# Kernel tuning notes

Hardware: AMD Instinct MI355X
Metric: run time of the kernel (lower is better)

The kernel has to match this reference:

```python
import jax, jax.numpy as jnp
import numpy as np

DIM = 512
HEADS = 16
WS = (2, 7, 7)
N = WS[0] * WS[1] * WS[2]  # 98
NW = 64  # number of windows in mask
B_ = 512  # num_windows * batch
HEAD_DIM = DIM // HEADS
SCALE = HEAD_DIM ** -0.5
TABLE = (2 * WS[0] - 1) * (2 * WS[1] - 1) * (2 * WS[2] - 1)  # 507


def _relative_position_index():
    # Faithful to the repo (note: middle coord is NOT multiplied by (2*Ww-1),
    # matching the source exactly).
    ct, ch, cw = np.arange(WS[0]), np.arange(WS[1]), np.arange(WS[2])
    coords = np.stack(np.meshgrid(ct, ch, cw, indexing='ij'))  # [3,Th,Tw,Tw]
    flat = coords.reshape(3, -1)  # [3,N]
    rel = flat[:, :, None] - flat[:, None, :]  # [3,N,N]
    rel = rel.transpose(1, 2, 0).copy()  # [N,N,3]
    rel[:, :, 0] += WS[0] - 1
    rel[:, :, 1] += WS[1] - 1
    rel[:, :, 2] += WS[2] - 1
    rel[:, :, 0] *= (2 * WS[1] - 1) * (2 * WS[2] - 1)
    return rel.sum(-1).astype(np.int32)  # [N,N]


def setup_inputs() -> dict:
    key = jax.random.key(0)
    ks = jax.random.split(key, 7)
    x = jax.random.normal(ks[0], (B_, N, DIM), dtype=jnp.float32)
    mask = jnp.zeros((NW, N, N), dtype=jnp.float32)
    qkv_w = jax.random.normal(ks[1], (3 * DIM, DIM), dtype=jnp.float32) * (DIM ** -0.5)
    qkv_b = jnp.zeros((3 * DIM,), dtype=jnp.float32)
    proj_w = jax.random.normal(ks[2], (DIM, DIM), dtype=jnp.float32) * (DIM ** -0.5)
    proj_b = jnp.zeros((DIM,), dtype=jnp.float32)
    bias_table = jax.random.normal(ks[3], (TABLE, HEADS), dtype=jnp.float32) * 0.02
    rel_index = jnp.asarray(_relative_position_index())
    return {"x": x, "mask": mask, "qkv_w": qkv_w, "qkv_b": qkv_b,
            "proj_w": proj_w, "proj_b": proj_b, "bias_table": bias_table,
            "rel_index": rel_index}


def reference(x, mask, qkv_w, qkv_b, proj_w, proj_b, bias_table, rel_index):
    Bw, n, c = x.shape
    # QKV projection -> [3, B_, H, N, hd]
    qkv = (x @ qkv_w.T + qkv_b).reshape(Bw, n, 3, HEADS, HEAD_DIM)
    qkv = qkv.transpose(2, 0, 3, 1, 4)
    q, k, v = qkv[0], qkv[1], qkv[2]
    attn = jnp.einsum('bhnd,bhmd->bhnm', q * SCALE, k)  # [B_,H,N,N]
    # Gathered relative position bias -> [H,N,N]
    bias = bias_table[rel_index.reshape(-1)].reshape(n, n, HEADS).transpose(2, 0, 1)
    attn = attn + bias[None]
    # Broadcast mask over batch groups of nW windows
    nW = mask.shape[0]
    attn = attn.reshape(Bw // nW, nW, HEADS, n, n) + mask[None, :, None]
    attn = attn.reshape(Bw, HEADS, n, n)
    attn = jax.nn.softmax(attn, axis=-1)
    out = jnp.einsum('bhnm,bhmd->bhnd', attn, v)
    out = out.transpose(0, 2, 1, 3).reshape(Bw, n, c)
    return out @ proj_w.T + proj_b
```

## Files before the change

### kernel.cpp

```cpp
#include <hip/hip_runtime.h>
#include <stdint.h>

#define HEADS 16
#define NTOK 98
#define HD 32
#define SCALE_Q 0.17677669529663687f

typedef __attribute__((ext_vector_type(4))) float floatx4;
typedef __attribute__((ext_vector_type(8))) short shortx8;

__device__ __forceinline__ unsigned short f2bf(float f) {
  union { float f; unsigned u; } v; v.f = f;
  unsigned r = v.u + 0x7fffu + ((v.u >> 16) & 1u);
  return (unsigned short)(r >> 16);
}
__device__ __forceinline__ float bf2f(unsigned short s) {
  union { unsigned u; float f; } v; v.u = ((unsigned)s) << 16;
  return v.f;
}

__device__ __forceinline__ void gload_lds16(const void* g, void* l) {
  __builtin_amdgcn_global_load_lds(
      (const __attribute__((address_space(1))) unsigned int*)g,
      (__attribute__((address_space(3))) unsigned int*)l, 16, 0, 0);
}

__global__ void convert_x_kernel(const float* __restrict__ x,
                                 unsigned short* __restrict__ xbf) {
  int idx = blockIdx.x * 256 + threadIdx.x;
  const float4 f0 = *(const float4*)(x + (size_t)idx * 8);
  const float4 f1 = *(const float4*)(x + (size_t)idx * 8 + 4);
  union { ushort us[8]; uint4 u4; } pk;
  pk.us[0] = f2bf(f0.x); pk.us[1] = f2bf(f0.y);
  pk.us[2] = f2bf(f0.z); pk.us[3] = f2bf(f0.w);
  pk.us[4] = f2bf(f1.x); pk.us[5] = f2bf(f1.y);
  pk.us[6] = f2bf(f1.z); pk.us[7] = f2bf(f1.w);
  *(uint4*)(xbf + (size_t)idx * 8) = pk.u4;
}

__global__ void convert_w_kernel(const float* __restrict__ qkv_w,
                                 const float* __restrict__ proj_w,
                                 unsigned short* __restrict__ wq,
                                 unsigned short* __restrict__ wp) {
  int idx = blockIdx.x * 256 + threadIdx.x;
  if (idx < 1536 * 512) wq[idx] = f2bf(qkv_w[idx]);
  if (idx < 512 * 512) wp[idx] = f2bf(proj_w[idx]);
}

__global__ void bmprep_kernel(const float* __restrict__ table,
                              const int* __restrict__ rel,
                              const float* __restrict__ mask,
                              unsigned short* __restrict__ biasF,
                              unsigned short* __restrict__ maskF) {
  int idx = blockIdx.x * 256 + threadIdx.x;
  if (idx < 229376) {
    int e = idx & 31, lane = (idx >> 5) & 63;
    int rest = idx >> 11;
    int mt = rest % 7, h = rest / 7;
    int nt = e >> 2, r = e & 3;
    int i = mt * 16 + ((lane >> 4) << 2) + r;
    int j = (nt << 4) + (lane & 15);
    int ii = i < NTOK ? i : 97, jj = j < NTOK ? j : 97;
    float v = (nt < 7) ? table[rel[ii * NTOK + jj] * HEADS + h] : 0.f;
    biasF[idx] = f2bf(v);
  } else {
    int t = idx - 229376;
    int e = t & 31, lane = (t >> 5) & 63;
    int rest = t >> 11;
    int mt = rest % 7, wdx = rest / 7;
    int nt = e >> 2, r = e & 3;
    int i = mt * 16 + ((lane >> 4) << 2) + r;
    int j = (nt << 4) + (lane & 15);
    float v;
    if (nt >= 7) v = 0.f;
    else if (j >= NTOK) v = -1e30f;
    else {
      int ii = i < NTOK ? i : 97;
      v = mask[wdx * (NTOK * NTOK) + ii * NTOK + j];
    }
    maskF[t] = f2bf(v);
  }
}

__global__ __launch_bounds__(512, 2)
void qkv_gemm_kernel(const unsigned short* __restrict__ xbf,
                     const unsigned short* __restrict__ wbf,
                     const float* __restrict__ qkv_b,
                     unsigned short* __restrict__ q_out,
                     unsigned short* __restrict__ k_out,
                     unsigned short* __restrict__ v_out) {
  __shared__ unsigned short As[3][128 * 32];
  __shared__ unsigned short Bs[3][256 * 32];
  const int tid = threadIdx.x;
  const int wave = tid >> 6, lane = tid & 63;
  const int m0 = blockIdx.x * 128, n0 = blockIdx.y * 256;
  const int wm = wave & 1, wn = wave >> 1;
  const int ln15 = lane & 15, qd = lane >> 4;
  const int bl_r = lane >> 2, bl_s = lane & 3;

  const int sg_st = bl_s ^ ((bl_r >> 1) & 3);
  const int swz_rd = (qd ^ ((ln15 >> 1) & 3)) * 8;

  const unsigned short* aG = xbf + (size_t)(m0 + wave * 16 + bl_r) * 512 + sg_st * 8;
  const unsigned short* bG0 = wbf + (size_t)(n0 + wave * 32 + bl_r) * 512 + sg_st * 8;
  const unsigned short* bG1 = wbf + (size_t)(n0 + wave * 32 + 16 + bl_r) * 512 + sg_st * 8;

#define QSTAGE(bufi, kk)                                                        \
  do {                                                                          \
    gload_lds16((const void*)(aG + (kk)), (void*)&As[bufi][wave * 512]);        \
    gload_lds16((const void*)(bG0 + (kk)), (void*)&Bs[bufi][wave * 1024]);      \
    gload_lds16((const void*)(bG1 + (kk)), (void*)&Bs[bufi][wave * 1024 + 512]);\
  } while (0)

  QSTAGE(0, 0);
  QSTAGE(1, 32);

  floatx4 acc[4][4] = {};
#pragma unroll
  for (int it = 0; it < 16; ++it) {
    if (it == 15) asm volatile("s_waitcnt vmcnt(0)" ::: "memory");
    else          asm volatile("s_waitcnt vmcnt(3)" ::: "memory");
    __builtin_amdgcn_sched_barrier(0);
    __builtin_amdgcn_s_barrier();
    __builtin_amdgcn_sched_barrier(0);
    if (it + 2 < 16) QSTAGE((it + 2) % 3, (it + 2) * 32);
    const unsigned short* Ab = As[it % 3];
    const unsigned short* Bb = Bs[it % 3];
    shortx8 afrag[4], bfrag[4];
#pragma unroll
    for (int mt = 0; mt < 4; ++mt)
      afrag[mt] = *(const shortx8*)&Ab[(wm * 64 + mt * 16 + ln15) * 32 + swz_rd];
#pragma unroll
    for (int nt = 0; nt < 4; ++nt)
      bfrag[nt] = *(const shortx8*)&Bb[(wn * 64 + nt * 16 + ln15) * 32 + swz_rd];
#pragma unroll
    for (int mt = 0; mt < 4; ++mt)
#pragma unroll
      for (int nt = 0; nt < 4; ++nt)
        acc[mt][nt] = __builtin_amdgcn_mfma_f32_16x16x32_bf16(
            afrag[mt], bfrag[nt], acc[mt][nt], 0, 0, 0);
  }
#undef QSTAGE

#pragma unroll
  for (int mt = 0; mt < 4; ++mt) {
#pragma unroll
    for (int r = 0; r < 4; ++r) {
      int grow = m0 + wm * 64 + mt * 16 + qd * 4 + r;
      unsigned b = (unsigned)grow / 98u;
      unsigned i = (unsigned)grow - b * 98u;
#pragma unroll
      for (int nt = 0; nt < 4; ++nt) {
        int col = n0 + wn * 64 + nt * 16 + ln15;
        float val = acc[mt][nt][r] + qkv_b[col];
        int which = col >> 9;
        int h = (col >> 5) & 15;
        int d = col & 31;
        size_t oidx = ((size_t)(b * 16 + h) * 98 + i) * 32 + d;
        if (which == 0)      q_out[oidx] = f2bf(val * SCALE_Q);
        else if (which == 1) k_out[oidx] = f2bf(val);
        else                 v_out[oidx] = f2bf(val);
      }
    }
  }
}

__global__ __launch_bounds__(448, 6)
void attn_kernel(const unsigned short* __restrict__ qg,
                 const unsigned short* __restrict__ kg,
                 const unsigned short* __restrict__ vg,
                 const unsigned short* __restrict__ biasF,
                 const unsigned short* __restrict__ maskF,
                 unsigned short* __restrict__ outg) {
  __shared__ __align__(16) unsigned short Vt[32 * 136];
  __shared__ __align__(16) unsigned short Ps[7][1928];
  const int tid = threadIdx.x;
  const int bh = blockIdx.x;
  const int b = bh >> 4, h = bh & 15, w = b & 63;
  const size_t base = (size_t)bh * (NTOK * HD);
  const int wave = tid >> 6, lane = tid & 63;
  const int ln15 = lane & 15, qd = lane >> 4;

  for (int idx = tid; idx < 544; idx += 448)
    ((uint4*)Vt)[idx] = make_uint4(0, 0, 0, 0);
  for (int idx = tid; idx < 1687; idx += 448)
    ((uint4*)Ps)[idx] = make_uint4(0, 0, 0, 0);
  __syncthreads();
  for (int t = tid; t < 392; t += 448) {
    int i = t >> 2, seg = t & 3;
    union { uint4 u4; unsigned short us[8]; } u;
    u.u4 = *(const uint4*)(vg + base + i * 32 + seg * 8);
    int d0 = seg * 8;
#pragma unroll
    for (int e0 = 0; e0 < 8; ++e0) {
      int e = (e0 + seg * 2) & 7;
      Vt[(d0 + e) * 136 + i] = u.us[e];
    }
  }
  __syncthreads();

  const int mt = wave;
  const shortx8* bB = (const shortx8*)(biasF + (((size_t)h * 7 + mt) * 64 + lane) * 32);
  const shortx8* mB = (const shortx8*)(maskF + (((size_t)w * 7 + mt) * 64 + lane) * 32);
  shortx8 bias_c[4], mask_c[4];
#pragma unroll
  for (int c = 0; c < 4; ++c) { bias_c[c] = bB[c]; mask_c[c] = mB[c]; }

  shortx8 af = *(const shortx8*)(qg + base + (mt * 16 + ln15) * 32 + qd * 8);
  floatx4 sacc[7];
#pragma unroll
  for (int nt = 0; nt < 7; ++nt) {
    shortx8 bf = *(const shortx8*)(kg + base + (nt * 16 + ln15) * 32 + qd * 8);
    floatx4 z = {};
    sacc[nt] = __builtin_amdgcn_mfma_f32_16x16x32_bf16(af, bf, z, 0, 0, 0);
  }
#pragma unroll
  for (int nt = 0; nt < 7; ++nt)
#pragma unroll
    for (int r = 0; r < 4; ++r) {
      int ee = nt * 4 + r, c = ee >> 3, el = ee & 7;
      sacc[nt][r] += bf2f((unsigned short)bias_c[c][el]) +
                     bf2f((unsigned short)mask_c[c][el]);
    }

  float linv[4];
#pragma unroll
  for (int r = 0; r < 4; ++r) {
    float mx = sacc[0][r];
#pragma unroll
    for (int nt = 1; nt < 7; ++nt) mx = fmaxf(mx, sacc[nt][r]);
#pragma unroll
    for (int off = 1; off < 16; off <<= 1)
      mx = fmaxf(mx, __shfl_xor(mx, off, 64));
    float sum = 0.f;
#pragma unroll
    for (int nt = 0; nt < 7; ++nt) {
      float p = __expf(sacc[nt][r] - mx);
      sacc[nt][r] = p;
      sum += p;
    }
#pragma unroll
    for (int off = 1; off < 16; off <<= 1) sum += __shfl_xor(sum, off, 64);
    linv[r] = 1.0f / sum;
  }

  unsigned short* Pw = Ps[wave];
#pragma unroll
  for (int nt = 0; nt < 7; ++nt)
#pragma unroll
    for (int r = 0; r < 4; ++r)
      Pw[(qd * 4 + r) * 120 + nt * 16 + ln15] = f2bf(sacc[nt][r]);

  floatx4 o0 = {}, o1 = {};
#pragma unroll
  for (int ks = 0; ks < 4; ++ks) {
    shortx8 ap = *(const shortx8*)&Pw[ln15 * 120 + ks * 32 + qd * 8];
    shortx8 bv0 = *(const shortx8*)&Vt[ln15 * 136 + ks * 32 + qd * 8];
    shortx8 bv1 = *(const shortx8*)&Vt[(16 + ln15) * 136 + ks * 32 + qd * 8];
    o0 = __builtin_amdgcn_mfma_f32_16x16x32_bf16(ap, bv0, o0, 0, 0, 0);
    o1 = __builtin_amdgcn_mfma_f32_16x16x32_bf16(ap, bv1, o1, 0, 0, 0);
  }
#pragma unroll
  for (int r = 0; r < 4; ++r) {
    int i = mt * 16 + qd * 4 + r;
    if (i < NTOK) {
      size_t ob = ((size_t)b * NTOK + i) * 512 + h * 32;
      outg[ob + ln15] = f2bf(o0[r] * linv[r]);
      outg[ob + 16 + ln15] = f2bf(o1[r] * linv[r]);
    }
  }
}

__global__ __launch_bounds__(512, 2)
void proj_gemm_kernel(const unsigned short* __restrict__ a,
                      const unsigned short* __restrict__ wbf,
                      const float* __restrict__ proj_b,
                      float* __restrict__ out) {
  __shared__ unsigned short As[3][128 * 32];
  __shared__ unsigned short Bs[3][256 * 32];
  const int tid = threadIdx.x;
  const int wave = tid >> 6, lane = tid & 63;
  const int m0 = blockIdx.x * 128, n0 = blockIdx.y * 256;
  const int wm = wave & 1, wn = wave >> 1;
  const int ln15 = lane & 15, qd = lane >> 4;
  const int bl_r = lane >> 2, bl_s = lane & 3;

  const int sg_st = bl_s ^ ((bl_r >> 1) & 3);
  const int swz_rd = (qd ^ ((ln15 >> 1) & 3)) * 8;

  const unsigned short* aG = a + (size_t)(m0 + wave * 16 + bl_r) * 512 + sg_st * 8;
  const unsigned short* bG0 = wbf + (size_t)(n0 + wave * 32 + bl_r) * 512 + sg_st * 8;
  const unsigned short* bG1 = wbf + (size_t)(n0 + wave * 32 + 16 + bl_r) * 512 + sg_st * 8;

#define PSTAGE(bufi, kk)                                                        \
  do {                                                                          \
    gload_lds16((const void*)(aG + (kk)), (void*)&As[bufi][wave * 512]);        \
    gload_lds16((const void*)(bG0 + (kk)), (void*)&Bs[bufi][wave * 1024]);      \
    gload_lds16((const void*)(bG1 + (kk)), (void*)&Bs[bufi][wave * 1024 + 512]);\
  } while (0)

  PSTAGE(0, 0);
  PSTAGE(1, 32);

  floatx4 acc[4][4] = {};
#pragma unroll
  for (int it = 0; it < 16; ++it) {
    if (it == 15) asm volatile("s_waitcnt vmcnt(0)" ::: "memory");
    else          asm volatile("s_waitcnt vmcnt(3)" ::: "memory");
    __builtin_amdgcn_sched_barrier(0);
    __builtin_amdgcn_s_barrier();
    __builtin_amdgcn_sched_barrier(0);
    if (it + 2 < 16) PSTAGE((it + 2) % 3, (it + 2) * 32);
    const unsigned short* Ab = As[it % 3];
    const unsigned short* Bb = Bs[it % 3];
    shortx8 afrag[4], bfrag[4];
#pragma unroll
    for (int mt = 0; mt < 4; ++mt)
      afrag[mt] = *(const shortx8*)&Ab[(wm * 64 + mt * 16 + ln15) * 32 + swz_rd];
#pragma unroll
    for (int nt = 0; nt < 4; ++nt)
      bfrag[nt] = *(const shortx8*)&Bb[(wn * 64 + nt * 16 + ln15) * 32 + swz_rd];
#pragma unroll
    for (int mt = 0; mt < 4; ++mt)
#pragma unroll
      for (int nt = 0; nt < 4; ++nt)
        acc[mt][nt] = __builtin_amdgcn_mfma_f32_16x16x32_bf16(
            afrag[mt], bfrag[nt], acc[mt][nt], 0, 0, 0);
  }
#undef PSTAGE

#pragma unroll
  for (int mt = 0; mt < 4; ++mt) {
#pragma unroll
    for (int r = 0; r < 4; ++r) {
      int grow = m0 + wm * 64 + mt * 16 + qd * 4 + r;
#pragma unroll
      for (int nt = 0; nt < 4; ++nt) {
        int col = n0 + wn * 64 + nt * 16 + ln15;
        out[(size_t)grow * 512 + col] = acc[mt][nt][r] + proj_b[col];
      }
    }
  }
}

extern "C" void kernel_launch(void* const* d_in, const int* in_sizes, int n_in,
                              void* d_out, int out_size, void* d_ws, size_t ws_size,
                              hipStream_t stream) {
  const float* x          = (const float*)d_in[0];
  const float* mask       = (const float*)d_in[1];
  const float* qkv_w      = (const float*)d_in[2];
  const float* qkv_b      = (const float*)d_in[3];
  const float* proj_w     = (const float*)d_in[4];
  const float* proj_b     = (const float*)d_in[5];
  const float* bias_table = (const float*)d_in[6];
  const int*   rel_index  = (const int*)d_in[7];
  float* out = (float*)d_out;

  char* ws = (char*)d_ws;
  unsigned short* ws_qkvw  = (unsigned short*)(ws + 0);
  unsigned short* ws_projw = (unsigned short*)(ws + 1572864);
  unsigned short* ws_biasF = (unsigned short*)(ws + 2097152);
  unsigned short* ws_maskF = (unsigned short*)(ws + 2555904);
  unsigned short* ws_q     = (unsigned short*)(ws + 4390912);
  unsigned short* ws_k     = (unsigned short*)(ws + 55771136);
  unsigned short* ws_v     = (unsigned short*)(ws + 107151360);
  unsigned short* ws_attn  = (unsigned short*)(ws + 158531584);
  unsigned short* ws_xbf   = ws_attn;

  hipLaunchKernelGGL(convert_x_kernel, dim3(12544), dim3(256), 0, stream,
                     x, ws_xbf);
  hipLaunchKernelGGL(convert_w_kernel, dim3(3072), dim3(256), 0, stream,
                     qkv_w, proj_w, ws_qkvw, ws_projw);
  hipLaunchKernelGGL(bmprep_kernel, dim3(4480), dim3(256), 0, stream,
                     bias_table, rel_index, mask, ws_biasF, ws_maskF);
  hipLaunchKernelGGL(qkv_gemm_kernel, dim3(392, 6), dim3(512), 0, stream,
                     ws_xbf, ws_qkvw, qkv_b, ws_q, ws_k, ws_v);
  hipLaunchKernelGGL(attn_kernel, dim3(8192), dim3(448), 0, stream,
                     ws_q, ws_k, ws_v, ws_biasF, ws_maskF, ws_attn);
  hipLaunchKernelGGL(proj_gemm_kernel, dim3(392, 2), dim3(512), 0, stream,
                     ws_attn, ws_projw, proj_b, out);
}
```

Measured before the change: 452.8 us.

## Remap GEMM block order per XCD, shrink proj tile, add MFMA priority hints

Both GEMMs switch to a 1D grid whose block index is remapped so each of the 8 XCDs gets a contiguous band of M rows, with all N tiles of a row band scheduled together for L2 reuse. The projection GEMM moves to a 128x128 tile with 256 threads and 3 blocks per CU, giving more blocks and better occupancy. The QKV epilogue hoists the q/k/v selection and scale out of the inner loop, and s_setprio raises wave priority around MFMA sections in the GEMMs and the attention kernel. Risks include changed L2 behaviour from the remap and a lower arithmetic intensity for the smaller projection tile.

```diff
diff --git a/kernel.cpp b/kernel.cpp
--- a/kernel.cpp
+++ b/kernel.cpp
@@ -93,7 +93,9 @@
   __shared__ unsigned short Bs[3][256 * 32];
   const int tid = threadIdx.x;
   const int wave = tid >> 6, lane = tid & 63;
-  const int m0 = blockIdx.x * 128, n0 = blockIdx.y * 256;
+  const int id = blockIdx.x;
+  const int xc = id & 7, tt = id >> 3;
+  const int m0 = (xc * 49 + tt / 6) * 128, n0 = (tt % 6) * 256;
   const int wm = wave & 1, wn = wave >> 1;
   const int ln15 = lane & 15, qd = lane >> 4;
   const int bl_r = lane >> 2, bl_s = lane & 3;
@@ -133,15 +135,21 @@
 #pragma unroll
     for (int nt = 0; nt < 4; ++nt)
       bfrag[nt] = *(const shortx8*)&Bb[(wn * 64 + nt * 16 + ln15) * 32 + swz_rd];
+    __builtin_amdgcn_s_setprio(1);
 #pragma unroll
     for (int mt = 0; mt < 4; ++mt)
 #pragma unroll
       for (int nt = 0; nt < 4; ++nt)
         acc[mt][nt] = __builtin_amdgcn_mfma_f32_16x16x32_bf16(
             afrag[mt], bfrag[nt], acc[mt][nt], 0, 0, 0);
+    __builtin_amdgcn_s_setprio(0);
   }
 #undef QSTAGE
 
+  const int which = n0 >> 9;
+  unsigned short* __restrict__ outp =
+      (which == 0) ? q_out : ((which == 1) ? k_out : v_out);
+  const float sc = (which == 0) ? SCALE_Q : 1.0f;
 #pragma unroll
   for (int mt = 0; mt < 4; ++mt) {
 #pragma unroll
@@ -152,14 +160,11 @@
 #pragma unroll
       for (int nt = 0; nt < 4; ++nt) {
         int col = n0 + wn * 64 + nt * 16 + ln15;
-        float val = acc[mt][nt][r] + qkv_b[col];
-        int which = col >> 9;
+        float val = (acc[mt][nt][r] + qkv_b[col]) * sc;
         int h = (col >> 5) & 15;
         int d = col & 31;
         size_t oidx = ((size_t)(b * 16 + h) * 98 + i) * 32 + d;
-        if (which == 0)      q_out[oidx] = f2bf(val * SCALE_Q);
-        else if (which == 1) k_out[oidx] = f2bf(val);
-        else                 v_out[oidx] = f2bf(val);
+        outp[oidx] = f2bf(val);
       }
     }
   }
@@ -208,12 +213,14 @@
 
   shortx8 af = *(const shortx8*)(qg + base + (mt * 16 + ln15) * 32 + qd * 8);
   floatx4 sacc[7];
+  __builtin_amdgcn_s_setprio(1);
 #pragma unroll
   for (int nt = 0; nt < 7; ++nt) {
     shortx8 bf = *(const shortx8*)(kg + base + (nt * 16 + ln15) * 32 + qd * 8);
     floatx4 z = {};
     sacc[nt] = __builtin_amdgcn_mfma_f32_16x16x32_bf16(af, bf, z, 0, 0, 0);
   }
+  __builtin_amdgcn_s_setprio(0);
 #pragma unroll
   for (int nt = 0; nt < 7; ++nt)
 #pragma unroll
@@ -252,6 +259,7 @@
       Pw[(qd * 4 + r) * 120 + nt * 16 + ln15] = f2bf(sacc[nt][r]);
 
   floatx4 o0 = {}, o1 = {};
+  __builtin_amdgcn_s_setprio(1);
 #pragma unroll
   for (int ks = 0; ks < 4; ++ks) {
     shortx8 ap = *(const shortx8*)&Pw[ln15 * 120 + ks * 32 + qd * 8];
@@ -260,6 +268,7 @@
     o0 = __builtin_amdgcn_mfma_f32_16x16x32_bf16(ap, bv0, o0, 0, 0, 0);
     o1 = __builtin_amdgcn_mfma_f32_16x16x32_bf16(ap, bv1, o1, 0, 0, 0);
   }
+  __builtin_amdgcn_s_setprio(0);
 #pragma unroll
   for (int r = 0; r < 4; ++r) {
     int i = mt * 16 + qd * 4 + r;
@@ -271,16 +280,18 @@
   }
 }
 
-__global__ __launch_bounds__(512, 2)
+__global__ __launch_bounds__(256, 3)
 void proj_gemm_kernel(const unsigned short* __restrict__ a,
                       const unsigned short* __restrict__ wbf,
                       const float* __restrict__ proj_b,
                       float* __restrict__ out) {
   __shared__ unsigned short As[3][128 * 32];
-  __shared__ unsigned short Bs[3][256 * 32];
+  __shared__ unsigned short Bs[3][128 * 32];
   const int tid = threadIdx.x;
   const int wave = tid >> 6, lane = tid & 63;
-  const int m0 = blockIdx.x * 128, n0 = blockIdx.y * 256;
+  const int id = blockIdx.x;
+  const int xc = id & 7, tt = id >> 3;
+  const int m0 = (xc * 49 + (tt >> 2)) * 128, n0 = (tt & 3) * 128;
   const int wm = wave & 1, wn = wave >> 1;
   const int ln15 = lane & 15, qd = lane >> 4;
   const int bl_r = lane >> 2, bl_s = lane & 3;
@@ -288,15 +299,17 @@
   const int sg_st = bl_s ^ ((bl_r >> 1) & 3);
   const int swz_rd = (qd ^ ((ln15 >> 1) & 3)) * 8;
 
-  const unsigned short* aG = a + (size_t)(m0 + wave * 16 + bl_r) * 512 + sg_st * 8;
+  const unsigned short* aG0 = a + (size_t)(m0 + wave * 32 + bl_r) * 512 + sg_st * 8;
+  const unsigned short* aG1 = aG0 + (size_t)16 * 512;
   const unsigned short* bG0 = wbf + (size_t)(n0 + wave * 32 + bl_r) * 512 + sg_st * 8;
-  const unsigned short* bG1 = wbf + (size_t)(n0 + wave * 32 + 16 + bl_r) * 512 + sg_st * 8;
-
-#define PSTAGE(bufi, kk)                                                        \
-  do {                                                                          \
-    gload_lds16((const void*)(aG + (kk)), (void*)&As[bufi][wave * 512]);        \
-    gload_lds16((const void*)(bG0 + (kk)), (void*)&Bs[bufi][wave * 1024]);      \
-    gload_lds16((const void*)(bG1 + (kk)), (void*)&Bs[bufi][wave * 1024 + 512]);\
+  const unsigned short* bG1 = bG0 + (size_t)16 * 512;
+
+#define PSTAGE(bufi, kk)                                                         \
+  do {                                                                           \
+    gload_lds16((const void*)(aG0 + (kk)), (void*)&As[bufi][wave * 1024]);       \
+    gload_lds16((const void*)(aG1 + (kk)), (void*)&As[bufi][wave * 1024 + 512]); \
+    gload_lds16((const void*)(bG0 + (kk)), (void*)&Bs[bufi][wave * 1024]);       \
+    gload_lds16((const void*)(bG1 + (kk)), (void*)&Bs[bufi][wave * 1024 + 512]); \
   } while (0)
 
   PSTAGE(0, 0);
@@ -306,7 +319,7 @@
 #pragma unroll
   for (int it = 0; it < 16; ++it) {
     if (it == 15) asm volatile("s_waitcnt vmcnt(0)" ::: "memory");
-    else          asm volatile("s_waitcnt vmcnt(3)" ::: "memory");
+    else          asm volatile("s_waitcnt vmcnt(4)" ::: "memory");
     __builtin_amdgcn_sched_barrier(0);
     __builtin_amdgcn_s_barrier();
     __builtin_amdgcn_sched_barrier(0);
@@ -320,12 +333,14 @@
 #pragma unroll
     for (int nt = 0; nt < 4; ++nt)
       bfrag[nt] = *(const shortx8*)&Bb[(wn * 64 + nt * 16 + ln15) * 32 + swz_rd];
+    __builtin_amdgcn_s_setprio(1);
 #pragma unroll
     for (int mt = 0; mt < 4; ++mt)
 #pragma unroll
       for (int nt = 0; nt < 4; ++nt)
         acc[mt][nt] = __builtin_amdgcn_mfma_f32_16x16x32_bf16(
             afrag[mt], bfrag[nt], acc[mt][nt], 0, 0, 0);
+    __builtin_amdgcn_s_setprio(0);
   }
 #undef PSTAGE
 
@@ -373,10 +388,10 @@
                      qkv_w, proj_w, ws_qkvw, ws_projw);
   hipLaunchKernelGGL(bmprep_kernel, dim3(4480), dim3(256), 0, stream,
                      bias_table, rel_index, mask, ws_biasF, ws_maskF);
-  hipLaunchKernelGGL(qkv_gemm_kernel, dim3(392, 6), dim3(512), 0, stream,
+  hipLaunchKernelGGL(qkv_gemm_kernel, dim3(2352), dim3(512), 0, stream,
                      ws_xbf, ws_qkvw, qkv_b, ws_q, ws_k, ws_v);
   hipLaunchKernelGGL(attn_kernel, dim3(8192), dim3(448), 0, stream,
                      ws_q, ws_k, ws_v, ws_biasF, ws_maskF, ws_attn);
-  hipLaunchKernelGGL(proj_gemm_kernel, dim3(392, 2), dim3(512), 0, stream,
+  hipLaunchKernelGGL(proj_gemm_kernel, dim3(1568), dim3(256), 0, stream,
                      ws_attn, ws_projw, proj_b, out);
 }
```

Result: faster. 426.7 us (-5.8%).
